# Kernel optimization log

Measured on AMD Instinct MI355X. Metric: run time of the kernel, lower is better.

## Reference

```python
import jax, jax.numpy as jnp
import numpy as np

H, C, PQ, PV, CZ, CS = 12, 16, 4, 8, 128, 384
W_C = (2.0 / (9.0 * PQ)) ** 0.5
INV_SQRT3 = 3.0 ** -0.5


def setup_inputs() -> dict:
    key = jax.random.key(0)
    ks = jax.random.split(key, 20)
    B, N = 2, 512
    s = jax.random.normal(ks[0], (B, N, CS), jnp.float32)
    z = jax.random.normal(ks[1], (B, N, N, CZ), jnp.float32)
    m = jax.random.normal(ks[2], (B, N, 3, 3), jnp.float32)
    rot, _ = jnp.linalg.qr(m)  # proper-ish rotations (orthonormal frames)
    trans = jax.random.normal(ks[3], (B, N, 3), jnp.float32)
    seq_mask = jnp.ones((B, N), jnp.float32)
    sc = 0.02
    params = {
        'Wq': jax.random.normal(ks[4], (CS, H * C)) * sc,
        'bq': jnp.zeros((H * C,)),
        'Wkv': jax.random.normal(ks[5], (CS, H * C * 2)) * sc,
        'bkv': jnp.zeros((H * C * 2,)),
        'Wb': jax.random.normal(ks[6], (CZ, H)) * sc,
        'bb': jnp.zeros((H,)),
        'Wqp': jax.random.normal(ks[7], (CS, 3 * PQ * H)) * sc,
        'bqp': jnp.zeros((3 * PQ * H,)),
        'Wkvp': jax.random.normal(ks[8], (CS, 3 * (PQ + PV) * H)) * sc,
        'bkvp': jnp.zeros((3 * (PQ + PV) * H,)),
        'gamma': jnp.zeros((H,)),
        'Wout': jax.random.normal(ks[9], ((CZ + C + PV * 4) * H, CS)) * sc,
        'bout': jnp.zeros((CS,)),
    }
    return dict(s=s, z=z, rot=rot, trans=trans, seq_mask=seq_mask, **params)


def reference(s, z, rot, trans, seq_mask, Wq, bq, Wkv, bkv, Wb, bb, Wqp, bqp, Wkvp, bkvp, gamma, Wout, bout):
    B, N, _ = s.shape
    # scalar q/k/v
    q = (s @ Wq + bq).reshape(B, N, H, C)
    kv = (s @ Wkv + bkv).reshape(B, N, H, 2 * C)
    k, v = kv[..., :C], kv[..., C:]
    qp = s @ Wqp + bqp                                   # (B,N,3*PQ*H)
    qp = jnp.stack(jnp.split(qp, 3, axis=-1), axis=-1)   # (B,N,PQ*H,3)
    qp = jnp.einsum('bixy,bipy->bipx', rot, qp) + trans[:, :, None, :]
    qp = qp.reshape(B, N, H, PQ, 3)
    # key/value points
    kvp = s @ Wkvp + bkvp
    kvp = jnp.stack(jnp.split(kvp, 3, axis=-1), axis=-1)  # (B,N,(PQ+PV)*H,3)
    kvp = jnp.einsum('bixy,bipy->bipx', rot, kvp) + trans[:, :, None, :]
    kvp = kvp.reshape(B, N, H, PQ + PV, 3)
    kp, vp = kvp[..., :PQ, :], kvp[..., PQ:, :]
    # attention logits: scalar term + pair bias + point-distance term
    bpair = (z @ Wb + bb).transpose(0, 3, 1, 2)          # (B,H,i,j)
    a = jnp.einsum('bihc,bjhc->bhij', q, k) * (3 * C) ** -0.5 + INV_SQRT3 * bpair
    d2 = jnp.sum((qp[:, :, None] - kp[:, None]) ** 2, axis=-1)   # (B,i,j,H,PQ)
    pa = -0.5 * jnp.sum(d2, axis=-1)                      # (B,i,j,H)
    head_w = jax.nn.softplus(gamma)
    pa = pa * (head_w * W_C * INV_SQRT3)
    a = a + pa.transpose(0, 3, 1, 2)
    mask_bias = 100000.0 * (seq_mask[:, :, None] * seq_mask[:, None, :] - 1.0)
    a = a + mask_bias[:, None, :, :]
    a = jax.nn.softmax(a, axis=-1)                        # (B,H,i,j)
    # outputs: scalar values, rotated points (inverse frame), pair features
    o = jnp.einsum('bhij,bjhc->bihc', a, v).reshape(B, N, H * C)
    op = jnp.einsum('bhij,bjhpx->bihpx', a, vp)           # (B,i,H,PV,3)
    op = jnp.einsum('biyx,bihpy->bihpx', rot, op - trans[:, :, None, None, :])  # R^T(p-t)
    onorm = jnp.maximum(jnp.sqrt(jnp.sum(op ** 2, axis=-1)), 1e-6).reshape(B, N, H * PV)
    op = op.reshape(B, N, H * PV, 3)
    opair = jnp.einsum('bhij,bijc->bihc', a, z).reshape(B, N, H * CZ)
    feat = jnp.concatenate([o, op[..., 0], op[..., 1], op[..., 2], onorm, opair], axis=-1)
    return feat @ Wout + bout
```

## Files before the change

### kernel.cpp

```cpp
#include <hip/hip_runtime.h>
#include <hip/hip_bf16.h>

constexpr int B = 2, N = 512, H = 12, C = 16, PQ = 4, PV = 8, CZ = 128, CS = 384;
constexpr int HC   = H * C;
constexpr int FEAT = (CZ + C + PV * 4) * H;
constexpr float QK_SCALE  = 0.14433756729740643f;
constexpr float INV_SQRT3 = 0.5773502691896258f;
constexpr float WC_IS3    = 0.13608276348795434f;

using f32x4 = __attribute__((ext_vector_type(4))) float;
using s16x8 = __attribute__((ext_vector_type(8))) short;

__device__ __forceinline__ short f2b(float f) {
    union { __hip_bfloat16 b; short s; } u;
    u.b = __float2bfloat16(f);
    return u.s;
}
__device__ __forceinline__ float b2f(short s) {
    union { short s; __hip_bfloat16 b; } u;
    u.s = s;
    return __bfloat162float(u.b);
}

__device__ __forceinline__ size_t kkps_idx(int row, int col) {
    return ((size_t)((row >> 4) * 12 + (col >> 5))) * 512
         + (size_t)(((row & 15) << 2) + ((col & 31) >> 3)) * 8 + (col & 7);
}

constexpr int RPB = 2;

__global__ __launch_bounds__(256) void k_proj(
    const float* __restrict__ s, const float* __restrict__ rot, const float* __restrict__ trans,
    const float* __restrict__ Wq, const float* __restrict__ bq,
    const float* __restrict__ Wkv, const float* __restrict__ bkv,
    const float* __restrict__ Wqp, const float* __restrict__ bqp,
    const float* __restrict__ Wkvp, const float* __restrict__ bkvp,
    const float* __restrict__ gamma, const float* __restrict__ bb,
    const float* __restrict__ Wout,
    short* __restrict__ qcw, short* __restrict__ kkpS,
    float* __restrict__ vw, float* __restrict__ vpw,
    short* __restrict__ pcw, float* __restrict__ auxw,
    short* __restrict__ WT)
{
    __shared__ float s_s[RPB][CS];
    __shared__ float rawqp_s[RPB][144];
    __shared__ float rawkvp_s[RPB][432];
    __shared__ float qrot_s[RPB][48][3];
    __shared__ float sq_s[RPB][48];
    __shared__ float R_s[RPB][9], T_s[RPB][3];
    const int t = threadIdx.x;
    const int bi0 = blockIdx.x * RPB;

    for (int idx = t; idx < RPB * CS / 4; idx += 256) {
        int r = idx / (CS / 4), k4 = idx % (CS / 4);
        ((float4*)s_s[r])[k4] = ((const float4*)(s + (size_t)(bi0 + r) * CS))[k4];
    }
    if (t < RPB * 9) R_s[t / 9][t % 9] = rot[bi0 * 9 + t];
    if (t < RPB * 3) T_s[t / 3][t % 3] = trans[bi0 * 3 + t];
    __syncthreads();

    for (int qd = t; qd < 288; qd += 256) {
        const int c = qd * 4;
        const float* Wp; int ldw; const float* bp;
        int seg;
        if (c < 192)      { Wp = Wq   + c;        ldw = 192; bp = bq + c;        seg = 0; }
        else if (c < 576) { Wp = Wkv  + (c - 192); ldw = 384; bp = bkv + (c - 192); seg = 1; }
        else if (c < 720) { Wp = Wqp  + (c - 576); ldw = 144; bp = bqp + (c - 576); seg = 2; }
        else              { Wp = Wkvp + (c - 720); ldw = 432; bp = bkvp + (c - 720); seg = 3; }
        float4 bv = *(const float4*)bp;
        float acc[RPB][4];
        #pragma unroll
        for (int r = 0; r < RPB; ++r) {
            acc[r][0] = bv.x; acc[r][1] = bv.y; acc[r][2] = bv.z; acc[r][3] = bv.w;
        }
        for (int k4 = 0; k4 < CS / 4; ++k4) {
            float4 sv[RPB];
            #pragma unroll
            for (int r = 0; r < RPB; ++r) sv[r] = *(const float4*)&s_s[r][k4 * 4];
            #pragma unroll
            for (int e = 0; e < 4; ++e) {
                float4 wv = *(const float4*)(Wp + (size_t)(k4 * 4 + e) * ldw);
                #pragma unroll
                for (int r = 0; r < RPB; ++r) {
                    float se = ((const float*)&sv[r])[e];
                    acc[r][0] += se * wv.x; acc[r][1] += se * wv.y;
                    acc[r][2] += se * wv.z; acc[r][3] += se * wv.w;
                }
            }
        }
        if (seg == 0) {
            #pragma unroll
            for (int r = 0; r < RPB; ++r) {
                short4 o = make_short4(f2b(QK_SCALE * acc[r][0]), f2b(QK_SCALE * acc[r][1]),
                                       f2b(QK_SCALE * acc[r][2]), f2b(QK_SCALE * acc[r][3]));
                *(short4*)&qcw[(size_t)(bi0 + r) * 192 + c] = o;
            }
        } else if (seg == 1) {
            int cc = c - 192, h = cc >> 5, w5 = cc & 31;
            if (w5 < 16) {
                int col = h * 16 + w5;
                #pragma unroll
                for (int r = 0; r < RPB; ++r) {
                    short4 o = make_short4(f2b(acc[r][0]), f2b(acc[r][1]),
                                           f2b(acc[r][2]), f2b(acc[r][3]));
                    *(short4*)&kkpS[kkps_idx(bi0 + r, col)] = o;
                }
            } else {
                #pragma unroll
                for (int r = 0; r < RPB; ++r) {
                    int row = bi0 + r;
                    *(float4*)&vw[(size_t)row * 192 + h * 16 + (w5 - 16)] =
                        (float4){acc[r][0], acc[r][1], acc[r][2], acc[r][3]};
                }
            }
        } else if (seg == 2) {
            #pragma unroll
            for (int r = 0; r < RPB; ++r)
                *(float4*)&rawqp_s[r][c - 576] = (float4){acc[r][0], acc[r][1], acc[r][2], acc[r][3]};
        } else {
            #pragma unroll
            for (int r = 0; r < RPB; ++r)
                *(float4*)&rawkvp_s[r][c - 720] = (float4){acc[r][0], acc[r][1], acc[r][2], acc[r][3]};
        }
    }
    __syncthreads();

    for (int idx = t; idx < RPB * 48; idx += 256) {
        int r = idx / 48, p = idx % 48;
        float y0 = rawqp_s[r][p], y1 = rawqp_s[r][48 + p], y2 = rawqp_s[r][96 + p];
        #pragma unroll
        for (int x = 0; x < 3; ++x)
            qrot_s[r][p][x] = T_s[r][x] + R_s[r][x * 3] * y0 + R_s[r][x * 3 + 1] * y1 + R_s[r][x * 3 + 2] * y2;
    }
    for (int idx = t; idx < RPB * 144; idx += 256) {
        int r = idx / 144, p = idx % 144, h = p / 12, pp = p % 12;
        float y0 = rawkvp_s[r][p], y1 = rawkvp_s[r][144 + p], y2 = rawkvp_s[r][288 + p];
        float vals[3]; float ss = 0.0f;
        #pragma unroll
        for (int x = 0; x < 3; ++x) {
            float v = T_s[r][x] + R_s[r][x * 3] * y0 + R_s[r][x * 3 + 1] * y1 + R_s[r][x * 3 + 2] * y2;
            vals[x] = v; ss += v * v;
        }
        int row = bi0 + r;
        if (pp < PQ) {
            #pragma unroll
            for (int x = 0; x < 3; ++x)
                kkpS[kkps_idx(row, 192 + h * 16 + pp * 3 + x)] = f2b(vals[x]);
            sq_s[r][h * 4 + pp] = ss;
        } else {
            #pragma unroll
            for (int x = 0; x < 3; ++x)
                vpw[(size_t)row * 288 + h * 24 + (pp - PQ) * 3 + x] = vals[x];
        }
    }
    __syncthreads();

    if (t < RPB * 12) {
        int r = t / 12, h = t % 12, row = bi0 + r;
        float g = gamma[h];
        float sp = fmaxf(g, 0.0f) + log1pf(expf(-fabsf(g)));
        float pac = -0.5f * sp * WC_IS3;
        float kpsq = sq_s[r][h * 4] + sq_s[r][h * 4 + 1] + sq_s[r][h * 4 + 2] + sq_s[r][h * 4 + 3];
        kkpS[kkps_idx(row, 192 + h * 16 + 12)] = f2b(kpsq);
        kkpS[kkps_idx(row, 192 + h * 16 + 13)] = 0;
        kkpS[kkps_idx(row, 192 + h * 16 + 14)] = 0;
        kkpS[kkps_idx(row, 192 + h * 16 + 15)] = 0;
        float qpsq = 0.0f;
        #pragma unroll
        for (int pq = 0; pq < 4; ++pq)
            #pragma unroll
            for (int x = 0; x < 3; ++x) {
                float qv = qrot_s[r][h * 4 + pq][x];
                qpsq += qv * qv;
                pcw[(size_t)row * 192 + h * 16 + pq * 3 + x] = f2b(-2.0f * pac * qv);
            }
        pcw[(size_t)row * 192 + h * 16 + 12] = f2b(pac);
        pcw[(size_t)row * 192 + h * 16 + 13] = 0;
        pcw[(size_t)row * 192 + h * 16 + 14] = 0;
        pcw[(size_t)row * 192 + h * 16 + 15] = 0;
        auxw[(size_t)row * 16 + h] = INV_SQRT3 * bb[h] + pac * qpsq;
    }
    if (t >= RPB * 12 && t < RPB * 16) {
        int r = (t - RPB * 12) >> 2, hh = 12 + ((t - RPB * 12) & 3);
        auxw[(size_t)(bi0 + r) * 16 + hh] = 0.0f;
    }

    short* tileb = (short*)&s_s[0][0];
    for (int tile = blockIdx.x; tile < 66 * 12; tile += 512) {
        const int k0 = (tile % 66) * 32;
        const int c0 = (tile / 66) * 32;
        __syncthreads();
        {
            int r = t >> 3, c4 = (t & 7) * 4;
            float4 v = *(const float4*)&Wout[(size_t)(k0 + r) * CS + c0 + c4];
            tileb[(c4 + 0) * 33 + r] = f2b(v.x);
            tileb[(c4 + 1) * 33 + r] = f2b(v.y);
            tileb[(c4 + 2) * 33 + r] = f2b(v.z);
            tileb[(c4 + 3) * 33 + r] = f2b(v.w);
        }
        __syncthreads();
        {
            int rr = t >> 3, k4 = (t & 7) * 4;
            short4 o = make_short4(tileb[rr * 33 + k4], tileb[rr * 33 + k4 + 1],
                                   tileb[rr * 33 + k4 + 2], tileb[rr * 33 + k4 + 3]);
            *(short4*)&WT[(size_t)(c0 + rr) * FEAT + k0 + k4] = o;
        }
    }
}

constexpr int PLS = 520;
constexpr int BSEL = 56;

#define LOADZ(BUF, PTR)                                                  \
    {                                                                    \
        _Pragma("unroll")                                                \
        for (int k4 = 0; k4 < 4; ++k4) {                                 \
            BUF[k4 * 2]     = *(const float4*)((PTR) + k4 * 32);         \
            BUF[k4 * 2 + 1] = *(const float4*)((PTR) + k4 * 32 + 4);     \
        }                                                                \
    }

#define STEP(CUR, NXT, JC, NZPTR, KPTR)                                            \
    {                                                                              \
        s16x8 kkpf[12];                                                            \
        _Pragma("unroll")                                                          \
        for (int kk = 0; kk < 12; ++kk)                                            \
            kkpf[kk] = *(const s16x8*)((KPTR) + kk * 512);                         \
        LOADZ(NXT, NZPTR);                                                         \
        f32x4 accA = (f32x4){0, 0, 0, 0}, accB = (f32x4){0, 0, 0, 0};              \
        _Pragma("unroll")                                                          \
        for (int kk = 0; kk < 4; ++kk) {                                           \
            float4 u0 = CUR[kk * 2], u1 = CUR[kk * 2 + 1];                         \
            s16x8 f;                                                               \
            f[0] = f2b(u0.x); f[1] = f2b(u0.y); f[2] = f2b(u0.z); f[3] = f2b(u0.w);\
            f[4] = f2b(u1.x); f[5] = f2b(u1.y); f[6] = f2b(u1.z); f[7] = f2b(u1.w);\
            s16x8 wb = *(const s16x8*)(bl + kk * 8);                               \
            accA = __builtin_amdgcn_mfma_f32_16x16x32_bf16(f, wb, accA, 0, 0, 0);  \
        }                                                                          \
        s16x8 qselr = *(const s16x8*)(bl + 32);                                    \
        s16x8 pselr = *(const s16x8*)(bl + 40);                                    \
        _Pragma("unroll")                                                          \
        for (int kk = 0; kk < 6; ++kk) {                                           \
            s16x8 bsel = (kk == half) ? qselr : z8;                                \
            accB = __builtin_amdgcn_mfma_f32_16x16x32_bf16(kkpf[kk], bsel, accB, 0, 0, 0); \
        }                                                                          \
        _Pragma("unroll")                                                          \
        for (int kk = 6; kk < 12; ++kk) {                                          \
            s16x8 bsel = ((kk - 6) == half) ? pselr : z8;                          \
            accA = __builtin_amdgcn_mfma_f32_16x16x32_bf16(kkpf[kk], bsel, accA, 0, 0, 0); \
        }                                                                          \
        f32x4 acc = accA + accB;                                                   \
        float4 m4 = *(const float4*)(mkp + (JC) * 16);                             \
        float lo[4]; float cm = -INFINITY;                                         \
        _Pragma("unroll")                                                          \
        for (int r = 0; r < 4; ++r) {                                              \
            lo[r] = acc[r] + constH + 100000.0f * (mask_i * ((const float*)&m4)[r] - 1.0f); \
            cm = fmaxf(cm, lo[r]);                                                 \
        }                                                                          \
        cm = fmaxf(cm, __shfl_xor(cm, 16, 64));                                    \
        cm = fmaxf(cm, __shfl_xor(cm, 32, 64));                                    \
        float p[4]; float ps = 0.0f;                                               \
        _Pragma("unroll")                                                          \
        for (int r = 0; r < 4; ++r) { p[r] = __expf(lo[r] - cm); ps += p[r]; }     \
        ps += __shfl_xor(ps, 16, 64);                                              \
        ps += __shfl_xor(ps, 32, 64);                                              \
        float mnew = fmaxf(m_run, cm);                                             \
        float sc = __expf(m_run - mnew);                                           \
        l_run = l_run * sc + ps * __expf(cm - mnew);                               \
        m_run = mnew;                                                              \
        if (lg == 0) mc_s[w][m15][JC] = cm;                                        \
        *(short4*)&P_lds[m15 * PLS + jw + (JC) * 16 + lg * 4] =                    \
            make_short4(f2b(p[0]), f2b(p[1]), f2b(p[2]), f2b(p[3]));               \
    }

__global__ __launch_bounds__(256) void k_attn2(
    const float* __restrict__ z, const float* __restrict__ rot, const float* __restrict__ trans,
    const float* __restrict__ seq_mask,
    const float* __restrict__ Wb,
    const short* __restrict__ qcw, const short* __restrict__ kkpS,
    const short* __restrict__ pcw, const float* __restrict__ auxw,
    const float* __restrict__ vw, const float* __restrict__ vpw,
    short* __restrict__ featb)
{
    __shared__ short P_lds[16 * PLS];
    __shared__ __align__(16) char ovl[7680];
    short* bsel_lds = (short*)ovl;
    float* ored_s   = (float*)ovl;
    float* opred_s  = (float*)(ovl + 3072);
    float* op_f     = (float*)(ovl + 6528);
    __shared__ float ml_s[4][16], ll_s[4][16], M_s[16], Linv_s[16];
    __shared__ float mc_s[4][16][8];
    __shared__ float R_s[9], T_s[3];

    const int t = threadIdx.x;
    const int w   = t >> 6;
    const int l   = t & 63;
    const int lg  = l >> 4;
    const int m15 = l & 15;
    const int bi  = blockIdx.x;
    const int b   = bi >> 9;
    const int i   = bi & (N - 1);

    if (t < 9) R_s[t] = rot[bi * 9 + t];
    if (t < 3) T_s[t] = trans[bi * 3 + t];

    const bool hv = (m15 < 12);
    const int hcl = hv ? m15 : 0;
    const int half = m15 >> 1;
    const float constH = auxw[(size_t)bi * 16 + m15];
    const float mask_i = seq_mask[bi];

    if (w == 0) {
        short* dst = &bsel_lds[l * BSEL];
        #pragma unroll
        for (int kk = 0; kk < 4; ++kk)
            #pragma unroll
            for (int e = 0; e < 8; ++e) {
                int c = kk * 32 + lg * 8 + e;
                dst[kk * 8 + e] = f2b(hv ? INV_SQRT3 * Wb[c * H + hcl] : 0.0f);
            }
        const bool selh = ((lg >> 1) == (m15 & 1));
        const s16x8 z8v = {0, 0, 0, 0, 0, 0, 0, 0};
        const short* qrow = qcw + (size_t)bi * 192 + hcl * 16;
        s16x8 qlo = *(const s16x8*)qrow;
        s16x8 qhi = *(const s16x8*)(qrow + 8);
        s16x8 q = (hv && selh) ? ((lg & 1) ? qhi : qlo) : z8v;
        const short* prow = pcw + (size_t)bi * 192 + hcl * 16;
        s16x8 plo = *(const s16x8*)prow;
        s16x8 phi = *(const s16x8*)(prow + 8);
        s16x8 p = (hv && selh) ? ((lg & 1) ? phi : plo) : z8v;
        *(s16x8*)(dst + 32) = q;
        *(s16x8*)(dst + 40) = p;
    }
    __syncthreads();

    float m_run = -INFINITY, l_run = 0.0f;

    const size_t zbase = ((size_t)b * N + i) * (size_t)(N * CZ);
    const int jw = w * 128;
    const float* zAp = z + zbase + (size_t)(jw + m15) * CZ + lg * 8;
    const short* kAp = kkpS + ((size_t)(b * 32 + (jw >> 4))) * 6144
                            + (size_t)(m15 * 4 + lg) * 8;
    const float* mkp = seq_mask + b * N + jw + lg * 4;
    const short* bl = &bsel_lds[l * BSEL];
    const s16x8 z8 = {0, 0, 0, 0, 0, 0, 0, 0};

    float4 bufA[8], bufB[8];
    LOADZ(bufA, zAp);

    for (int jc2 = 0; jc2 < 8; jc2 += 2) {
        STEP(bufA, bufB, jc2, zAp + 16 * CZ, kAp);
        kAp += 6144;
        STEP(bufB, bufA, jc2 + 1,
             (jc2 == 6) ? (zAp + 16 * CZ) : (zAp + 32 * CZ), kAp);
        kAp += 6144;
        zAp += 32 * CZ;
    }

    if (lg == 0) { ml_s[w][m15] = m_run; ll_s[w][m15] = l_run; }
    __syncthreads();
    if (t < 16) {
        float M = ml_s[0][t];
        M = fmaxf(M, ml_s[1][t]); M = fmaxf(M, ml_s[2][t]); M = fmaxf(M, ml_s[3][t]);
        float Lt = 0.0f;
        #pragma unroll
        for (int ww = 0; ww < 4; ++ww) Lt += ll_s[ww][t] * __expf(ml_s[ww][t] - M);
        M_s[t] = M;
        Linv_s[t] = 1.0f / Lt;
    }
    __syncthreads();

    {
        const int h = t >> 4, j0t = (t & 15) * 32;
        const int wv = j0t >> 7;
        const float Li = Linv_s[h], Mh = M_s[h];
        #pragma unroll
        for (int k = 0; k < 4; ++k) {
            const int lc = ((j0t & 127) >> 4) + (k >> 1);
            const float sS = __expf(mc_s[wv][h][lc] - Mh) * Li;
            s16x8 v = *(const s16x8*)&P_lds[h * PLS + j0t + k * 8];
            s16x8 o;
            #pragma unroll
            for (int e = 0; e < 8; ++e) o[e] = f2b(b2f(v[e]) * sS);
            *(s16x8*)&P_lds[h * PLS + j0t + k * 8] = o;
        }
    }
    __syncthreads();

    short* F = featb + (size_t)bi * FEAT;

    f32x4 oa0 = (f32x4){0, 0, 0, 0}, oa1 = (f32x4){0, 0, 0, 0};
    const int c0 = w * 32;
    #pragma unroll 4
    for (int kk = 0; kk < 16; ++kk) {
        s16x8 af = *(const s16x8*)&P_lds[m15 * PLS + kk * 32 + lg * 8];
        const float* zb = z + zbase + (size_t)(kk * 32 + lg * 8) * CZ + c0 + m15;
        s16x8 b0f, b1f;
        #pragma unroll
        for (int e = 0; e < 8; ++e) {
            b0f[e] = f2b(zb[(size_t)e * CZ]);
            b1f[e] = f2b(zb[(size_t)e * CZ + 16]);
        }
        oa0 = __builtin_amdgcn_mfma_f32_16x16x32_bf16(af, b0f, oa0, 0, 0, 0);
        oa1 = __builtin_amdgcn_mfma_f32_16x16x32_bf16(af, b1f, oa1, 0, 0, 0);
    }
    #pragma unroll
    for (int r = 0; r < 4; ++r) {
        int h = lg * 4 + r;
        if (h < 12) {
            F[576 + h * 128 + c0 + m15]      = f2b(oa0[r]);
            F[576 + h * 128 + c0 + 16 + m15] = f2b(oa1[r]);
        }
    }

    if (t < 192) {
        const int c4 = t % 48, jg = t / 48;
        const int h = c4 >> 2;
        const short* Pr = &P_lds[h * PLS + jg * 128];
        const float* vb = vw + ((size_t)b * N + jg * 128) * 192 + c4 * 4;
        f32x4 a = (f32x4){0, 0, 0, 0};
        #pragma unroll 2
        for (int q = 0; q < 16; ++q) {
            s16x8 pv = *(const s16x8*)(Pr + q * 8);
            #pragma unroll
            for (int e = 0; e < 8; ++e) {
                float4 v4 = *(const float4*)(vb + (size_t)(q * 8 + e) * 192);
                float pj = b2f(pv[e]);
                a[0] += pj * v4.x; a[1] += pj * v4.y; a[2] += pj * v4.z; a[3] += pj * v4.w;
            }
        }
        *(f32x4*)&ored_s[jg * 192 + c4 * 4] = a;
    }

    if (t < 216) {
        const int c4 = t % 72, jg = t / 72;
        const int h = c4 / 6;
        const int j0g = (jg == 0) ? 0 : (jg == 1 ? 176 : 352);
        const int nq = (jg == 2) ? 20 : 22;
        const short* Pr = &P_lds[h * PLS + j0g];
        const float* vb = vpw + ((size_t)b * N + j0g) * 288 + c4 * 4;
        f32x4 a = (f32x4){0, 0, 0, 0};
        #pragma unroll 2
        for (int q = 0; q < nq; ++q) {
            s16x8 pv = *(const s16x8*)(Pr + q * 8);
            #pragma unroll
            for (int e = 0; e < 8; ++e) {
                float4 v4 = *(const float4*)(vb + (size_t)(q * 8 + e) * 288);
                float pj = b2f(pv[e]);
                a[0] += pj * v4.x; a[1] += pj * v4.y; a[2] += pj * v4.z; a[3] += pj * v4.w;
            }
        }
        *(f32x4*)&opred_s[jg * 288 + c4 * 4] = a;
    }
    __syncthreads();

    if (t < 192)
        F[t] = f2b(ored_s[t] + ored_s[192 + t] + ored_s[384 + t] + ored_s[576 + t]);
    if (t < 72) {
        #pragma unroll
        for (int x = 0; x < 4; ++x) {
            int rv = t * 4 + x;
            op_f[rv] = opred_s[rv] + opred_s[288 + rv] + opred_s[576 + rv];
        }
    }
    __syncthreads();

    if (t < 96) {
        float o0 = op_f[t * 3 + 0] - T_s[0];
        float o1 = op_f[t * 3 + 1] - T_s[1];
        float o2 = op_f[t * 3 + 2] - T_s[2];
        float n2 = 0.0f;
        #pragma unroll
        for (int x = 0; x < 3; ++x) {
            float rx = R_s[0 * 3 + x] * o0 + R_s[1 * 3 + x] * o1 + R_s[2 * 3 + x] * o2;
            F[HC + 96 * x + t] = f2b(rx);
            n2 += rx * rx;
        }
        F[480 + t] = f2b(fmaxf(sqrtf(n2), 1e-6f));
    }
}

__global__ __launch_bounds__(256) void k_out(
    const short* __restrict__ featb, const short* __restrict__ WT,
    const float* __restrict__ bout, float* __restrict__ out)
{
    __shared__ short A_s[32 * 40];
    __shared__ short B_s[32 * 40];
    const int t = threadIdx.x;
    const int w   = t >> 6;
    const int l   = t & 63;
    const int lg  = l >> 4;
    const int m15 = l & 15;
    const int wm = w >> 1, wn = w & 1;
    const int bm = (blockIdx.x / 12) * 32;
    const int bn = (blockIdx.x % 12) * 32;

    f32x4 acc = (f32x4){0, 0, 0, 0};

    const int sr = (t & 127) >> 2;
    const int sk = (t & 3) * 8;

    s16x8 rS;
    if (t < 128) rS = *(const s16x8*)&featb[(size_t)(bm + sr) * FEAT + sk];
    else         rS = *(const s16x8*)&WT[(size_t)(bn + sr) * FEAT + sk];

    for (int k0 = 0; k0 < FEAT; k0 += 32) {
        __syncthreads();
        if (t < 128) *(s16x8*)&A_s[sr * 40 + sk] = rS;
        else         *(s16x8*)&B_s[sr * 40 + sk] = rS;
        __syncthreads();

        const int kn = k0 + 32;
        if (kn < FEAT) {
            if (t < 128) rS = *(const s16x8*)&featb[(size_t)(bm + sr) * FEAT + kn + sk];
            else         rS = *(const s16x8*)&WT[(size_t)(bn + sr) * FEAT + kn + sk];
        }

        s16x8 af = *(const s16x8*)&A_s[(wm * 16 + m15) * 40 + lg * 8];
        s16x8 bf = *(const s16x8*)&B_s[(wn * 16 + m15) * 40 + lg * 8];
        acc = __builtin_amdgcn_mfma_f32_16x16x32_bf16(af, bf, acc, 0, 0, 0);
    }

    {
        int col = bn + wn * 16 + m15;
        float bo = bout[col];
        #pragma unroll
        for (int r = 0; r < 4; ++r) {
            int row = bm + wm * 16 + lg * 4 + r;
            out[(size_t)row * CS + col] = acc[r] + bo;
        }
    }
}

extern "C" void kernel_launch(void* const* d_in, const int* in_sizes, int n_in,
                              void* d_out, int out_size, void* d_ws, size_t ws_size,
                              hipStream_t stream)
{
    const float* s     = (const float*)d_in[0];
    const float* z     = (const float*)d_in[1];
    const float* rot   = (const float*)d_in[2];
    const float* trans = (const float*)d_in[3];
    const float* mask  = (const float*)d_in[4];
    const float* Wq    = (const float*)d_in[5];
    const float* bq    = (const float*)d_in[6];
    const float* Wkv   = (const float*)d_in[7];
    const float* bkv   = (const float*)d_in[8];
    const float* Wb    = (const float*)d_in[9];
    const float* bb    = (const float*)d_in[10];
    const float* Wqp   = (const float*)d_in[11];
    const float* bqp   = (const float*)d_in[12];
    const float* Wkvp  = (const float*)d_in[13];
    const float* bkvp  = (const float*)d_in[14];
    const float* gamma = (const float*)d_in[15];
    const float* Wout  = (const float*)d_in[16];
    const float* bout  = (const float*)d_in[17];

    char* wsb = (char*)d_ws;
    short* featb = (short*)wsb;
    float* vw    = (float*)(wsb + 4325376);
    float* vpw   = (float*)(wsb + 5111808);
    float* auxw  = (float*)(wsb + 6291456);
    short* qcw   = (short*)(wsb + 6356992);
    short* pcw   = (short*)(wsb + 6750208);
    short* kkpS  = (short*)(wsb + 7143424);
    short* WT    = (short*)(wsb + 7929856);

    hipLaunchKernelGGL(k_proj, dim3(B * N / RPB), dim3(256), 0, stream,
                       s, rot, trans, Wq, bq, Wkv, bkv, Wqp, bqp, Wkvp, bkvp,
                       gamma, bb, Wout, qcw, kkpS, vw, vpw, pcw, auxw, WT);
    hipLaunchKernelGGL(k_attn2, dim3(B * N), dim3(256), 0, stream,
                       z, rot, trans, mask, Wb, qcw, kkpS, pcw, auxw, vw, vpw, featb);
    hipLaunchKernelGGL(k_out, dim3(384), dim3(256), 0, stream,
                       featb, WT, bout, (float*)d_out);
}
```

Baseline: 255.7 us.

## Split fused attention kernel into separate logits/softmax and PV kernels

```diff
diff --git a/kernel.cpp b/kernel.cpp
--- a/kernel.cpp
+++ b/kernel.cpp
@@ -273,24 +273,17 @@
             make_short4(f2b(p[0]), f2b(p[1]), f2b(p[2]), f2b(p[3]));               \
     }
 
-__global__ __launch_bounds__(256) void k_attn2(
-    const float* __restrict__ z, const float* __restrict__ rot, const float* __restrict__ trans,
-    const float* __restrict__ seq_mask,
+__global__ __launch_bounds__(256) void k_logits(
+    const float* __restrict__ z, const float* __restrict__ seq_mask,
     const float* __restrict__ Wb,
     const short* __restrict__ qcw, const short* __restrict__ kkpS,
     const short* __restrict__ pcw, const float* __restrict__ auxw,
-    const float* __restrict__ vw, const float* __restrict__ vpw,
-    short* __restrict__ featb)
+    short* __restrict__ Pg)
 {
     __shared__ short P_lds[16 * PLS];
-    __shared__ __align__(16) char ovl[7680];
-    short* bsel_lds = (short*)ovl;
-    float* ored_s   = (float*)ovl;
-    float* opred_s  = (float*)(ovl + 3072);
-    float* op_f     = (float*)(ovl + 6528);
+    __shared__ __align__(16) short bsel_lds[64 * BSEL];
     __shared__ float ml_s[4][16], ll_s[4][16], M_s[16], Linv_s[16];
     __shared__ float mc_s[4][16][8];
-    __shared__ float R_s[9], T_s[3];
 
     const int t = threadIdx.x;
     const int w   = t >> 6;
@@ -300,9 +293,6 @@
     const int bi  = blockIdx.x;
     const int b   = bi >> 9;
     const int i   = bi & (N - 1);
-
-    if (t < 9) R_s[t] = rot[bi * 9 + t];
-    if (t < 3) T_s[t] = trans[bi * 3 + t];
 
     const bool hv = (m15 < 12);
     const int hcl = hv ? m15 : 0;
@@ -374,6 +364,7 @@
         const int h = t >> 4, j0t = (t & 15) * 32;
         const int wv = j0t >> 7;
         const float Li = Linv_s[h], Mh = M_s[h];
+        short* dst = Pg + (size_t)bi * 8192 + h * 512 + j0t;
         #pragma unroll
         for (int k = 0; k < 4; ++k) {
             const int lc = ((j0t & 127) >> 4) + (k >> 1);
@@ -382,18 +373,44 @@
             s16x8 o;
             #pragma unroll
             for (int e = 0; e < 8; ++e) o[e] = f2b(b2f(v[e]) * sS);
-            *(s16x8*)&P_lds[h * PLS + j0t + k * 8] = o;
-        }
-    }
-    __syncthreads();
-
+            *(s16x8*)(dst + k * 8) = o;
+        }
+    }
+}
+
+__global__ __launch_bounds__(256) void k_pv(
+    const float* __restrict__ z, const float* __restrict__ rot, const float* __restrict__ trans,
+    const short* __restrict__ Pg,
+    const float* __restrict__ vw, const float* __restrict__ vpw,
+    short* __restrict__ featb)
+{
+    __shared__ float ored_s[4 * 192];
+    __shared__ float opred_s[3 * 288];
+    __shared__ float op_f[288];
+    __shared__ float R_s[9], T_s[3];
+
+    const int t = threadIdx.x;
+    const int w   = t >> 6;
+    const int l   = t & 63;
+    const int lg  = l >> 4;
+    const int m15 = l & 15;
+    const int bi  = blockIdx.x;
+    const int b   = bi >> 9;
+    const int i   = bi & (N - 1);
+
+    if (t < 9) R_s[t] = rot[bi * 9 + t];
+    if (t < 3) T_s[t] = trans[bi * 3 + t];
+    __syncthreads();
+
+    const short* Pw = Pg + (size_t)bi * 8192;
+    const size_t zbase = ((size_t)b * N + i) * (size_t)(N * CZ);
     short* F = featb + (size_t)bi * FEAT;
 
     f32x4 oa0 = (f32x4){0, 0, 0, 0}, oa1 = (f32x4){0, 0, 0, 0};
     const int c0 = w * 32;
     #pragma unroll 4
     for (int kk = 0; kk < 16; ++kk) {
-        s16x8 af = *(const s16x8*)&P_lds[m15 * PLS + kk * 32 + lg * 8];
+        s16x8 af = *(const s16x8*)(Pw + m15 * 512 + kk * 32 + lg * 8);
         const float* zb = z + zbase + (size_t)(kk * 32 + lg * 8) * CZ + c0 + m15;
         s16x8 b0f, b1f;
         #pragma unroll
@@ -416,7 +433,7 @@
     if (t < 192) {
         const int c4 = t % 48, jg = t / 48;
         const int h = c4 >> 2;
-        const short* Pr = &P_lds[h * PLS + jg * 128];
+        const short* Pr = Pw + h * 512 + jg * 128;
         const float* vb = vw + ((size_t)b * N + jg * 128) * 192 + c4 * 4;
         f32x4 a = (f32x4){0, 0, 0, 0};
         #pragma unroll 2
@@ -437,7 +454,7 @@
         const int h = c4 / 6;
         const int j0g = (jg == 0) ? 0 : (jg == 1 ? 176 : 352);
         const int nq = (jg == 2) ? 20 : 22;
-        const short* Pr = &P_lds[h * PLS + j0g];
+        const short* Pr = Pw + h * 512 + j0g;
         const float* vb = vpw + ((size_t)b * N + j0g) * 288 + c4 * 4;
         f32x4 a = (f32x4){0, 0, 0, 0};
         #pragma unroll 2
@@ -564,12 +581,15 @@
     short* pcw   = (short*)(wsb + 6750208);
     short* kkpS  = (short*)(wsb + 7143424);
     short* WT    = (short*)(wsb + 7929856);
+    short* Pg    = (short*)(wsb + 9551872);
 
     hipLaunchKernelGGL(k_proj, dim3(B * N / RPB), dim3(256), 0, stream,
                        s, rot, trans, Wq, bq, Wkv, bkv, Wqp, bqp, Wkvp, bkvp,
                        gamma, bb, Wout, qcw, kkpS, vw, vpw, pcw, auxw, WT);
-    hipLaunchKernelGGL(k_attn2, dim3(B * N), dim3(256), 0, stream,
-                       z, rot, trans, mask, Wb, qcw, kkpS, pcw, auxw, vw, vpw, featb);
+    hipLaunchKernelGGL(k_logits, dim3(B * N), dim3(256), 0, stream,
+                       z, mask, Wb, qcw, kkpS, pcw, auxw, Pg);
+    hipLaunchKernelGGL(k_pv, dim3(B * N), dim3(256), 0, stream,
+                       z, rot, trans, Pg, vw, vpw, featb);
     hipLaunchKernelGGL(k_out, dim3(384), dim3(256), 0, stream,
                        featb, WT, bout, (float*)d_out);
 }
```

Result: slower. 291.4 us (+14.0%).
